# Performance work log

Measured on AMD Instinct MI355X. Metric: run time of the kernel, lower is better.

Reference implementation:

```python
import jax, jax.numpy as jnp
import numpy as np

CELL_DIM = 64
FIELD_SIZE = 1.0

def setup_inputs() -> dict:
    key = jax.random.key(0)
    k1, k2 = jax.random.split(key)
    x = jax.random.normal(k1, (8192, CELL_DIM), dtype=jnp.float32)
    placeCells = jax.random.normal(k2, (512, CELL_DIM), dtype=jnp.float32)
    return {"x": x, "placeCells": placeCells}

def reference(x, placeCells):
    # states: (N, cellDim)
    states = x.reshape(-1, CELL_DIM)
    # broadcast L1 distance to every codebook cell: (N, numCells)
    l1 = jnp.sum(jnp.abs(states[:, None, :] - placeCells[None, :, :]), axis=-1)
    dists_squared = l1 * l1
    unnormalized = -dists_squared / (2.0 * FIELD_SIZE * FIELD_SIZE)
    return jax.nn.softmax(unnormalized, axis=1)
```

## Files before the change

kernel.cpp:

```cpp
#include <hip/hip_runtime.h>

#define DIM    64
#define NCELLS 512
#define CC     256
#define KC     32
#define ROWS_PER_BLOCK 8
#define NROWS  8192

__global__ __launch_bounds__(256, 4)
void placecells_kernel(const float* __restrict__ x,
                       const float* __restrict__ pc,
                       float* __restrict__ out)
{
    __shared__ float pcT[KC * CC];

    const int tid = (int)threadIdx.x;
    const int l   = tid & 63;
    const int w   = __builtin_amdgcn_readfirstlane(tid >> 6);
    const int rowBase = (int)blockIdx.x * ROWS_PER_BLOCK + w * 2;

    float4 a00{0,0,0,0}, a10{0,0,0,0};
    float4 a01{0,0,0,0}, a11{0,0,0,0};

    auto stage = [&](int cc, int kc) {
        #pragma unroll
        for (int i = 0; i < 8; ++i) {
            int idx = i * 256 + tid;
            int cl  = idx >> 3;
            int k4  = idx & 7;
            float4 v = *(const float4*)(pc + (cc * CC + cl) * DIM + kc * KC + k4 * 4);
            int pq = (cl >> 2) ^ k4;
            float* p = &pcT[(k4 * 4) * CC + pq * 4 + (cl & 3)];
            p[0 * CC] = v.x;
            p[1 * CC] = v.y;
            p[2 * CC] = v.z;
            p[3 * CC] = v.w;
        }
    };

    auto compute = [&](int kc, float4& A0, float4& A1) {
        #pragma unroll
        for (int k4 = 0; k4 < 8; ++k4) {
            float4 xv0 = *(const float4*)(x + (rowBase + 0) * DIM + kc * KC + k4 * 4);
            float4 xv1 = *(const float4*)(x + (rowBase + 1) * DIM + kc * KC + k4 * 4);
            const int pq4 = (l ^ k4) * 4;
            #pragma unroll
            for (int j = 0; j < 4; ++j) {
                float4 pv = *(const float4*)(&pcT[(k4 * 4 + j) * CC + pq4]);
                float x0 = (j == 0) ? xv0.x : (j == 1) ? xv0.y : (j == 2) ? xv0.z : xv0.w;
                float x1 = (j == 0) ? xv1.x : (j == 1) ? xv1.y : (j == 2) ? xv1.z : xv1.w;
                A0.x += fabsf(x0 - pv.x); A0.y += fabsf(x0 - pv.y);
                A0.z += fabsf(x0 - pv.z); A0.w += fabsf(x0 - pv.w);
                A1.x += fabsf(x1 - pv.x); A1.y += fabsf(x1 - pv.y);
                A1.z += fabsf(x1 - pv.z); A1.w += fabsf(x1 - pv.w);
            }
        }
    };

    stage(0, 0); __syncthreads();
    compute(0, a00, a10);
    __syncthreads(); stage(0, 1); __syncthreads();
    compute(1, a00, a10);
    __syncthreads(); stage(1, 0); __syncthreads();
    compute(0, a01, a11);
    __syncthreads(); stage(1, 1); __syncthreads();
    compute(1, a01, a11);

    auto finish_row = [&](float4 a, float4 b, int r) {
        float mn = fminf(fminf(fminf(a.x, a.y), fminf(a.z, a.w)),
                         fminf(fminf(b.x, b.y), fminf(b.z, b.w)));
        #pragma unroll
        for (int off = 32; off > 0; off >>= 1)
            mn = fminf(mn, __shfl_xor(mn, off, 64));
        float m2 = mn * mn;

        float e0 = __expf(0.5f * (m2 - a.x * a.x));
        float e1 = __expf(0.5f * (m2 - a.y * a.y));
        float e2 = __expf(0.5f * (m2 - a.z * a.z));
        float e3 = __expf(0.5f * (m2 - a.w * a.w));
        float e4 = __expf(0.5f * (m2 - b.x * b.x));
        float e5 = __expf(0.5f * (m2 - b.y * b.y));
        float e6 = __expf(0.5f * (m2 - b.z * b.z));
        float e7 = __expf(0.5f * (m2 - b.w * b.w));
        float s = ((e0 + e1) + (e2 + e3)) + ((e4 + e5) + (e6 + e7));
        #pragma unroll
        for (int off = 32; off > 0; off >>= 1)
            s += __shfl_xor(s, off, 64);
        float inv = 1.0f / s;

        float* orow = out + (size_t)(rowBase + r) * NCELLS;
        *(float4*)(orow + 4 * l)      = make_float4(e0 * inv, e1 * inv, e2 * inv, e3 * inv);
        *(float4*)(orow + CC + 4 * l) = make_float4(e4 * inv, e5 * inv, e6 * inv, e7 * inv);
    };
    finish_row(a00, a01, 0);
    finish_row(a10, a11, 1);
}

extern "C" void kernel_launch(void* const* d_in, const int* in_sizes, int n_in,
                              void* d_out, int out_size, void* d_ws, size_t ws_size,
                              hipStream_t stream)
{
    const float* x  = (const float*)d_in[0];
    const float* pc = (const float*)d_in[1];
    float* out = (float*)d_out;
    placecells_kernel<<<dim3(NROWS / ROWS_PER_BLOCK), dim3(256), 0, stream>>>(x, pc, out);
}
```

Before: 81.29 us.

## Keep place-cell rows in registers, one cell per thread, block-wide softmax reduction

Each of 512 threads now holds one full place-cell vector (64 floats) in registers, replacing the LDS-transposed codebook tiles. The x rows are read through uniform scalar/broadcast loads, four rows at a time. Because a row's 512 cells are now spread across 8 wavefronts, the softmax min and sum become cross-wave reductions through shared memory with two barriers per 4-row group. This removes the LDS staging traffic and its barriers, but adds 64+ registers per thread, which limits occupancy, plus extra block syncs. The codebook is also reloaded from global for every 16-row block.

Result: slower. 86.54 us (+6.5%).

```diff
diff --git a/kernel.cpp b/kernel.cpp
--- a/kernel.cpp
+++ b/kernel.cpp
@@ -2,98 +2,123 @@
 
 #define DIM    64
 #define NCELLS 512
-#define CC     256
-#define KC     32
-#define ROWS_PER_BLOCK 8
+#define ROWS_PER_BLOCK 16
 #define NROWS  8192
 
-__global__ __launch_bounds__(256, 4)
+#define CSTEP(pv, kk) \
+    a0 += fabsf(xr0[kk] - (pv)); \
+    a1 += fabsf(xr1[kk] - (pv)); \
+    a2 += fabsf(xr2[kk] - (pv)); \
+    a3 += fabsf(xr3[kk] - (pv));
+
+#define QSTEP(Pq, q) \
+    CSTEP((Pq).x, 4*(q)+0) \
+    CSTEP((Pq).y, 4*(q)+1) \
+    CSTEP((Pq).z, 4*(q)+2) \
+    CSTEP((Pq).w, 4*(q)+3)
+
+__global__ __launch_bounds__(512, 4)
 void placecells_kernel(const float* __restrict__ x,
                        const float* __restrict__ pc,
                        float* __restrict__ out)
 {
-    __shared__ float pcT[KC * CC];
+    __shared__ float redMin[2][8][4];
+    __shared__ float redSum[2][8][4];
 
     const int tid = (int)threadIdx.x;
     const int l   = tid & 63;
-    const int w   = __builtin_amdgcn_readfirstlane(tid >> 6);
-    const int rowBase = (int)blockIdx.x * ROWS_PER_BLOCK + w * 2;
+    const int w   = tid >> 6;
+    const int rowBase = (int)blockIdx.x * ROWS_PER_BLOCK;
 
-    float4 a00{0,0,0,0}, a10{0,0,0,0};
-    float4 a01{0,0,0,0}, a11{0,0,0,0};
+    const float* pcl = pc + tid * DIM;
+    float4 P0  = *(const float4*)(pcl +  0);
+    float4 P1  = *(const float4*)(pcl +  4);
+    float4 P2  = *(const float4*)(pcl +  8);
+    float4 P3  = *(const float4*)(pcl + 12);
+    float4 P4  = *(const float4*)(pcl + 16);
+    float4 P5  = *(const float4*)(pcl + 20);
+    float4 P6  = *(const float4*)(pcl + 24);
+    float4 P7  = *(const float4*)(pcl + 28);
+    float4 P8  = *(const float4*)(pcl + 32);
+    float4 P9  = *(const float4*)(pcl + 36);
+    float4 P10 = *(const float4*)(pcl + 40);
+    float4 P11 = *(const float4*)(pcl + 44);
+    float4 P12 = *(const float4*)(pcl + 48);
+    float4 P13 = *(const float4*)(pcl + 52);
+    float4 P14 = *(const float4*)(pcl + 56);
+    float4 P15 = *(const float4*)(pcl + 60);
 
-    auto stage = [&](int cc, int kc) {
+    auto wred_min = [&](float v) {
         #pragma unroll
-        for (int i = 0; i < 8; ++i) {
-            int idx = i * 256 + tid;
-            int cl  = idx >> 3;
-            int k4  = idx & 7;
-            float4 v = *(const float4*)(pc + (cc * CC + cl) * DIM + kc * KC + k4 * 4);
-            int pq = (cl >> 2) ^ k4;
-            float* p = &pcT[(k4 * 4) * CC + pq * 4 + (cl & 3)];
-            p[0 * CC] = v.x;
-            p[1 * CC] = v.y;
-            p[2 * CC] = v.z;
-            p[3 * CC] = v.w;
-        }
+        for (int off = 32; off > 0; off >>= 1) v = fminf(v, __shfl_xor(v, off, 64));
+        return v;
+    };
+    auto wred_sum = [&](float v) {
+        #pragma unroll
+        for (int off = 32; off > 0; off >>= 1) v += __shfl_xor(v, off, 64);
+        return v;
     };
 
-    auto compute = [&](int kc, float4& A0, float4& A1) {
+    auto do_group = [&](int g, int par) {
+        const float* xr0 = x + (size_t)(rowBase + 4 * g) * DIM;
+        const float* xr1 = xr0 + DIM;
+        const float* xr2 = xr1 + DIM;
+        const float* xr3 = xr2 + DIM;
+        float a0 = 0.f, a1 = 0.f, a2 = 0.f, a3 = 0.f;
+
+        QSTEP(P0,  0)  QSTEP(P1,  1)  QSTEP(P2,  2)  QSTEP(P3,  3)
+        QSTEP(P4,  4)  QSTEP(P5,  5)  QSTEP(P6,  6)  QSTEP(P7,  7)
+        QSTEP(P8,  8)  QSTEP(P9,  9)  QSTEP(P10, 10) QSTEP(P11, 11)
+        QSTEP(P12, 12) QSTEP(P13, 13) QSTEP(P14, 14) QSTEP(P15, 15)
+
+        float m0 = wred_min(a0), m1 = wred_min(a1);
+        float m2 = wred_min(a2), m3 = wred_min(a3);
+        if (l == 0) {
+            redMin[par][w][0] = m0; redMin[par][w][1] = m1;
+            redMin[par][w][2] = m2; redMin[par][w][3] = m3;
+        }
+        __syncthreads();
+        float M0 = redMin[par][0][0], M1 = redMin[par][0][1];
+        float M2 = redMin[par][0][2], M3 = redMin[par][0][3];
         #pragma unroll
-        for (int k4 = 0; k4 < 8; ++k4) {
-            float4 xv0 = *(const float4*)(x + (rowBase + 0) * DIM + kc * KC + k4 * 4);
-            float4 xv1 = *(const float4*)(x + (rowBase + 1) * DIM + kc * KC + k4 * 4);
-            const int pq4 = (l ^ k4) * 4;
-            #pragma unroll
-            for (int j = 0; j < 4; ++j) {
-                float4 pv = *(const float4*)(&pcT[(k4 * 4 + j) * CC + pq4]);
-                float x0 = (j == 0) ? xv0.x : (j == 1) ? xv0.y : (j == 2) ? xv0.z : xv0.w;
-                float x1 = (j == 0) ? xv1.x : (j == 1) ? xv1.y : (j == 2) ? xv1.z : xv1.w;
-                A0.x += fabsf(x0 - pv.x); A0.y += fabsf(x0 - pv.y);
-                A0.z += fabsf(x0 - pv.z); A0.w += fabsf(x0 - pv.w);
-                A1.x += fabsf(x1 - pv.x); A1.y += fabsf(x1 - pv.y);
-                A1.z += fabsf(x1 - pv.z); A1.w += fabsf(x1 - pv.w);
-            }
+        for (int ww = 1; ww < 8; ++ww) {
+            M0 = fminf(M0, redMin[par][ww][0]);
+            M1 = fminf(M1, redMin[par][ww][1]);
+            M2 = fminf(M2, redMin[par][ww][2]);
+            M3 = fminf(M3, redMin[par][ww][3]);
         }
+        float e0 = __expf(0.5f * (M0 * M0 - a0 * a0));
+        float e1 = __expf(0.5f * (M1 * M1 - a1 * a1));
+        float e2 = __expf(0.5f * (M2 * M2 - a2 * a2));
+        float e3 = __expf(0.5f * (M3 * M3 - a3 * a3));
+        float s0 = wred_sum(e0), s1 = wred_sum(e1);
+        float s2 = wred_sum(e2), s3 = wred_sum(e3);
+        if (l == 0) {
+            redSum[par][w][0] = s0; redSum[par][w][1] = s1;
+            redSum[par][w][2] = s2; redSum[par][w][3] = s3;
+        }
+        __syncthreads();
+        float S0 = redSum[par][0][0], S1 = redSum[par][0][1];
+        float S2 = redSum[par][0][2], S3 = redSum[par][0][3];
+        #pragma unroll
+        for (int ww = 1; ww < 8; ++ww) {
+            S0 += redSum[par][ww][0];
+            S1 += redSum[par][ww][1];
+            S2 += redSum[par][ww][2];
+            S3 += redSum[par][ww][3];
+        }
+        float i0 = 1.0f / S0, i1 = 1.0f / S1, i2 = 1.0f / S2, i3 = 1.0f / S3;
+
+        out[(size_t)(rowBase + 4 * g + 0) * NCELLS + tid] = e0 * i0;
+        out[(size_t)(rowBase + 4 * g + 1) * NCELLS + tid] = e1 * i1;
+        out[(size_t)(rowBase + 4 * g + 2) * NCELLS + tid] = e2 * i2;
+        out[(size_t)(rowBase + 4 * g + 3) * NCELLS + tid] = e3 * i3;
     };
 
-    stage(0, 0); __syncthreads();
-    compute(0, a00, a10);
-    __syncthreads(); stage(0, 1); __syncthreads();
-    compute(1, a00, a10);
-    __syncthreads(); stage(1, 0); __syncthreads();
-    compute(0, a01, a11);
-    __syncthreads(); stage(1, 1); __syncthreads();
-    compute(1, a01, a11);
-
-    auto finish_row = [&](float4 a, float4 b, int r) {
-        float mn = fminf(fminf(fminf(a.x, a.y), fminf(a.z, a.w)),
-                         fminf(fminf(b.x, b.y), fminf(b.z, b.w)));
-        #pragma unroll
-        for (int off = 32; off > 0; off >>= 1)
-            mn = fminf(mn, __shfl_xor(mn, off, 64));
-        float m2 = mn * mn;
-
-        float e0 = __expf(0.5f * (m2 - a.x * a.x));
-        float e1 = __expf(0.5f * (m2 - a.y * a.y));
-        float e2 = __expf(0.5f * (m2 - a.z * a.z));
-        float e3 = __expf(0.5f * (m2 - a.w * a.w));
-        float e4 = __expf(0.5f * (m2 - b.x * b.x));
-        float e5 = __expf(0.5f * (m2 - b.y * b.y));
-        float e6 = __expf(0.5f * (m2 - b.z * b.z));
-        float e7 = __expf(0.5f * (m2 - b.w * b.w));
-        float s = ((e0 + e1) + (e2 + e3)) + ((e4 + e5) + (e6 + e7));
-        #pragma unroll
-        for (int off = 32; off > 0; off >>= 1)
-            s += __shfl_xor(s, off, 64);
-        float inv = 1.0f / s;
-
-        float* orow = out + (size_t)(rowBase + r) * NCELLS;
-        *(float4*)(orow + 4 * l)      = make_float4(e0 * inv, e1 * inv, e2 * inv, e3 * inv);
-        *(float4*)(orow + CC + 4 * l) = make_float4(e4 * inv, e5 * inv, e6 * inv, e7 * inv);
-    };
-    finish_row(a00, a01, 0);
-    finish_row(a10, a11, 1);
+    do_group(0, 0);
+    do_group(1, 1);
+    do_group(2, 0);
+    do_group(3, 1);
 }
 
 extern "C" void kernel_launch(void* const* d_in, const int* in_sizes, int n_in,
@@ -103,5 +128,5 @@
     const float* x  = (const float*)d_in[0];
     const float* pc = (const float*)d_in[1];
     float* out = (float*)d_out;
-    placecells_kernel<<<dim3(NROWS / ROWS_PER_BLOCK), dim3(256), 0, stream>>>(x, pc, out);
+    placecells_kernel<<<dim3(NROWS / ROWS_PER_BLOCK), dim3(512), 0, stream>>>(x, pc, out);
 }
```
